# Kernel optimization log

Hardware: AMD Instinct MI355X
Metric: run time of the kernel (lower is better)

## Reference

```python
import jax, jax.numpy as jnp
import numpy as np

EMBED_DIM = 1024
HEADS = 16
D_HEAD = EMBED_DIM // HEADS
B, S = 4, 2048


def setup_inputs() -> dict:
    key = jax.random.key(0)
    ks = jax.random.split(key, 7)
    scale = 1.0 / np.sqrt(EMBED_DIM)
    inp = {
        "key": jax.random.normal(ks[0], (B, S, EMBED_DIM), jnp.float32),
        "query": jax.random.normal(ks[1], (B, S, EMBED_DIM), jnp.float32),
        "value": jax.random.normal(ks[2], (B, S, EMBED_DIM), jnp.float32),
        # causal boolean mask, broadcastable to [B, H, S, S]
        "mask": jnp.tril(jnp.ones((S, S), dtype=bool))[None, None, :, :] * jnp.ones((B, 1, 1, 1), dtype=bool),
        # nn.Linear weights, stored torch-style as [out_features, in_features]
        "Wq": jax.random.normal(ks[3], (EMBED_DIM, EMBED_DIM), jnp.float32) * scale,
        "Wk": jax.random.normal(ks[4], (EMBED_DIM, EMBED_DIM), jnp.float32) * scale,
        "Wv": jax.random.normal(ks[5], (EMBED_DIM, EMBED_DIM), jnp.float32) * scale,
        "Wo": jax.random.normal(ks[6], (EMBED_DIM, EMBED_DIM), jnp.float32) * scale,
    }
    return inp


def reference(key, query, value, mask, Wq, Wk, Wv, Wo):
    # projections (nn.Linear, bias=False): x @ W.T
    q = query @ Wq.T                                    # [B,S,E]
    k = key @ Wk.T
    v = value @ Wv.T
    # split heads -> [B,H,S,d]
    def split(x):
        return x.reshape(B, S, HEADS, D_HEAD).transpose(0, 2, 1, 3)
    q, k, v = split(q), split(k), split(v)
    # scaled dot-product scores [B,H,S,S]
    scores = jnp.einsum("bhqd,bhkd->bhqk", q, k) / np.sqrt(D_HEAD).astype(np.float32)
    scores = jnp.where(mask, scores, jnp.float32(-1e9))
    attn = jax.nn.softmax(scores, axis=-1)
    # attention output, merge heads
    out = jnp.einsum("bhqk,bhkd->bhqd", attn, v)        # [B,H,S,d]
    out = out.transpose(0, 2, 1, 3).reshape(B, S, EMBED_DIM)
    return out @ Wo.T
```

## Files before the change

kernel.cpp:

```cpp
#include <hip/hip_runtime.h>

#define SEQ 2048
#define EMBED 1024
#define DHEAD 64

typedef _Float16 h8 __attribute__((ext_vector_type(8)));
typedef _Float16 h4 __attribute__((ext_vector_type(4)));
typedef float f4 __attribute__((ext_vector_type(4)));
typedef unsigned int u32;

__device__ __forceinline__ void gload_lds16(const void* g, void* l) {
    __builtin_amdgcn_global_load_lds(
        (const __attribute__((address_space(1))) u32*)g,
        (__attribute__((address_space(3))) u32*)l, 16, 0, 0);
}

__global__ __launch_bounds__(256) void cvt_f16(
    const float* __restrict__ q, const float* __restrict__ k, const float* __restrict__ v,
    const float* __restrict__ wq, const float* __restrict__ wk, const float* __restrict__ wv,
    const float* __restrict__ wo,
    _Float16* __restrict__ q16, _Float16* __restrict__ k16, _Float16* __restrict__ v16,
    _Float16* __restrict__ wq16, _Float16* __restrict__ wk16, _Float16* __restrict__ wv16,
    _Float16* __restrict__ wo16)
{
    int bid = blockIdx.x;
    const float* src;
    _Float16* dst;
    float scale = 1.0f;
    size_t base;
    if (bid < 24576) {
        int seg = bid >> 13;
        base = (size_t)(bid & 8191) * 1024 + threadIdx.x * 4;
        src = seg == 0 ? q : seg == 1 ? k : v;
        dst = seg == 0 ? q16 : seg == 1 ? k16 : v16;
    } else {
        int wb = bid - 24576;
        int seg = wb >> 10;
        base = (size_t)(wb & 1023) * 1024 + threadIdx.x * 4;
        src = seg == 0 ? wq : seg == 1 ? wk : seg == 2 ? wv : wo;
        dst = seg == 0 ? wq16 : seg == 1 ? wk16 : seg == 2 ? wv16 : wo16;
        if (seg == 0) scale = 0.18033688011112042f;
    }
    float4 x = *(const float4*)(src + base);
    h4 y = { (_Float16)(x.x * scale), (_Float16)(x.y * scale),
             (_Float16)(x.z * scale), (_Float16)(x.w * scale) };
    *(h4*)(dst + base) = y;
}

__device__ __forceinline__ void gemm_core(const _Float16* __restrict__ A, const _Float16* __restrict__ W,
                                          int m0, int n0, int tid,
                                          _Float16* As, _Float16* Bs, f4 acc[4][4])
{
    const int lane = tid & 63, wave = tid >> 6;
    const int t16 = lane & 15, quad = lane >> 4;
    const int wm = (wave >> 1) * 64, wn = (wave & 1) * 64;
    const int wb = wave * 64;
    const int u0 = tid, u1 = tid + 256;
    const int r0 = u0 >> 2, c0 = u0 & 3;
    const int r1 = u1 >> 2, c1 = u1 & 3;
    const _Float16* ga0 = A + (size_t)(m0 + r0) * 1024 + c0 * 8;
    const _Float16* ga1 = A + (size_t)(m0 + r1) * 1024 + c1 * 8;
    const _Float16* gb0 = W + (size_t)(n0 + r0) * 1024 + c0 * 8;
    const _Float16* gb1 = W + (size_t)(n0 + r1) * 1024 + c1 * 8;
    _Float16* la0 = As + wb * 8;
    _Float16* la1 = As + (256 + wb) * 8;
    _Float16* lb0 = Bs + wb * 8;
    _Float16* lb1 = Bs + (256 + wb) * 8;

    for (int k0 = 0; k0 < 1024; k0 += 32) {
        __syncthreads();
        gload_lds16(ga0 + k0, la0);
        gload_lds16(ga1 + k0, la1);
        gload_lds16(gb0 + k0, lb0);
        gload_lds16(gb1 + k0, lb1);
        __syncthreads();
        h8 af[4], bf[4];
#pragma unroll
        for (int i = 0; i < 4; ++i)
            af[i] = *(const h8*)(As + (wm + i * 16 + t16) * 32 + quad * 8);
#pragma unroll
        for (int j = 0; j < 4; ++j)
            bf[j] = *(const h8*)(Bs + (wn + j * 16 + t16) * 32 + quad * 8);
#pragma unroll
        for (int i = 0; i < 4; ++i)
#pragma unroll
            for (int j = 0; j < 4; ++j)
                acc[i][j] = __builtin_amdgcn_mfma_f32_16x16x32_f16(af[i], bf[j], acc[i][j], 0, 0, 0);
    }
}

__global__ __launch_bounds__(256) void proj_qkv(
    const _Float16* __restrict__ q16, const _Float16* __restrict__ k16, const _Float16* __restrict__ v16,
    const _Float16* __restrict__ Wq, const _Float16* __restrict__ Wk, const _Float16* __restrict__ Wv,
    _Float16* __restrict__ Qh, _Float16* __restrict__ Kh, _Float16* __restrict__ Vt)
{
    __shared__ _Float16 As[4096], Bs[4096];
    const int tid = threadIdx.x;
    const int z = blockIdx.z;
    const _Float16 *A, *W;
    int m0, n0;
    if (z == 2) { A = Wv; W = v16; m0 = blockIdx.y * 128; n0 = blockIdx.x * 128; }
    else if (z == 0) { A = q16; W = Wq; m0 = blockIdx.x * 128; n0 = blockIdx.y * 128; }
    else { A = k16; W = Wk; m0 = blockIdx.x * 128; n0 = blockIdx.y * 128; }

    f4 acc[4][4];
    const f4 z4 = {0.f, 0.f, 0.f, 0.f};
#pragma unroll
    for (int i = 0; i < 4; ++i)
#pragma unroll
        for (int j = 0; j < 4; ++j) acc[i][j] = z4;

    gemm_core(A, W, m0, n0, tid, As, Bs, acc);

    const int lane = tid & 63, wave = tid >> 6;
    const int t16 = lane & 15, quad = lane >> 4;
    const int wm = (wave >> 1) * 64, wn = (wave & 1) * 64;
#pragma unroll
    for (int i = 0; i < 4; ++i)
#pragma unroll
        for (int j = 0; j < 4; ++j)
#pragma unroll
            for (int reg = 0; reg < 4; ++reg) {
                int gm = m0 + wm + i * 16 + quad * 4 + reg;
                int gn = n0 + wn + j * 16 + t16;
                float vv = acc[i][j][reg];
                if (z < 2) {
                    int b = gm >> 11, s = gm & 2047, h = gn >> 6, dd = gn & 63;
                    _Float16* dst = (z == 0) ? Qh : Kh;
                    dst[(((size_t)(b * 16 + h) * SEQ) + s) * DHEAD + dd] = (_Float16)vv;
                } else {
                    int h = gm >> 6, dd = gm & 63, b = gn >> 11, s = gn & 2047;
                    Vt[(((size_t)(b * 16 + h) * DHEAD) + dd) * SEQ + s] = (_Float16)vv;
                }
            }
}

__global__ __launch_bounds__(256) void attn2(
    const _Float16* __restrict__ Qh, const _Float16* __restrict__ Kh,
    const _Float16* __restrict__ Vt, _Float16* __restrict__ Ob)
{
    __shared__ _Float16 KVs[2][2][4096];
    __shared__ float Ps[64 * 68];
    const int tid = threadIdx.x;
    const int lane = tid & 63, wave = tid >> 6;
    const int t16 = lane & 15, quad = lane >> 4;
    const int bh = blockIdx.x;
    const int b = bh >> 4, h = bh & 15;
    const int qb = (gridDim.y - 1) - blockIdx.y;
    const int q0 = qb * 64;
    const int nt = qb + 1;

    const _Float16* Qp = Qh + (size_t)bh * SEQ * DHEAD;
    const _Float16* Kp = Kh + (size_t)bh * SEQ * DHEAD;
    const _Float16* Vp = Vt + (size_t)bh * DHEAD * SEQ;

    h8 qf0 = *(const h8*)(Qp + (size_t)(q0 + wave * 16 + t16) * 64 + quad * 8);
    h8 qf1 = *(const h8*)(Qp + (size_t)(q0 + wave * 16 + t16) * 64 + 32 + quad * 8);

    const int wb = wave * 64;
    const int sr0 = tid >> 3,          sc0 = (tid & 7) ^ (sr0 & 7);
    const int sr1 = (tid + 256) >> 3,  sc1 = ((tid + 256) & 7) ^ (sr1 & 7);

#define STAGE(jt, bufi)                                                                     \
    do {                                                                                    \
        gload_lds16(Kp + (size_t)((jt) * 64 + sr0) * 64 + sc0 * 8, &KVs[bufi][0][wb * 8]);  \
        gload_lds16(Kp + (size_t)((jt) * 64 + sr1) * 64 + sc1 * 8, &KVs[bufi][0][(256 + wb) * 8]); \
        gload_lds16(Vp + (size_t)sr0 * SEQ + (jt) * 64 + sc0 * 8, &KVs[bufi][1][wb * 8]);   \
        gload_lds16(Vp + (size_t)sr1 * SEQ + (jt) * 64 + sc1 * 8, &KVs[bufi][1][(256 + wb) * 8]); \
    } while (0)

    STAGE(0, 0);
    __syncthreads();

    float m_r[4] = {-1e30f, -1e30f, -1e30f, -1e30f};
    float l_r[4] = {0.f, 0.f, 0.f, 0.f};
    f4 o_acc[4];
    const f4 z4 = {0.f, 0.f, 0.f, 0.f};
#pragma unroll
    for (int dt = 0; dt < 4; ++dt) o_acc[dt] = z4;

    for (int jt = 0; jt < nt; ++jt) {
        const int buf = jt & 1;
        if (jt + 1 < nt) STAGE(jt + 1, buf ^ 1);
        const _Float16* Ks = KVs[buf][0];
        const _Float16* Vs = KVs[buf][1];

        f4 s_acc[4];
#pragma unroll
        for (int j4 = 0; j4 < 4; ++j4) s_acc[j4] = z4;
#pragma unroll
        for (int j4 = 0; j4 < 4; ++j4) {
            int row = j4 * 16 + t16, rx = row & 7;
            h8 kf0 = *(const h8*)(Ks + (row * 8 + (quad ^ rx)) * 8);
            h8 kf1 = *(const h8*)(Ks + (row * 8 + ((quad + 4) ^ rx)) * 8);
            s_acc[j4] = __builtin_amdgcn_mfma_f32_16x16x32_f16(qf0, kf0, s_acc[j4], 0, 0, 0);
            s_acc[j4] = __builtin_amdgcn_mfma_f32_16x16x32_f16(qf1, kf1, s_acc[j4], 0, 0, 0);
        }

        if (jt == nt - 1) {
#pragma unroll
            for (int j4 = 0; j4 < 4; ++j4) {
                int jg = jt * 64 + j4 * 16 + t16;
#pragma unroll
                for (int reg = 0; reg < 4; ++reg) {
                    int ig = q0 + wave * 16 + quad * 4 + reg;
                    if (jg > ig) s_acc[j4][reg] = -1e30f;
                }
            }
        }

        float mrow[4];
#pragma unroll
        for (int reg = 0; reg < 4; ++reg)
            mrow[reg] = fmaxf(fmaxf(s_acc[0][reg], s_acc[1][reg]),
                              fmaxf(s_acc[2][reg], s_acc[3][reg]));
#pragma unroll
        for (int off = 1; off < 16; off <<= 1)
#pragma unroll
            for (int reg = 0; reg < 4; ++reg)
                mrow[reg] = fmaxf(mrow[reg], __shfl_xor(mrow[reg], off, 64));

        float alpha[4];
#pragma unroll
        for (int reg = 0; reg < 4; ++reg) {
            float mn = fmaxf(m_r[reg], mrow[reg]);
            alpha[reg] = __builtin_amdgcn_exp2f(m_r[reg] - mn);
            m_r[reg] = mn;
        }
        float rsum[4] = {0.f, 0.f, 0.f, 0.f};
#pragma unroll
        for (int j4 = 0; j4 < 4; ++j4)
#pragma unroll
            for (int reg = 0; reg < 4; ++reg) {
                float p = __builtin_amdgcn_exp2f(s_acc[j4][reg] - m_r[reg]);
                s_acc[j4][reg] = p;
                rsum[reg] += p;
            }
#pragma unroll
        for (int off = 1; off < 16; off <<= 1)
#pragma unroll
            for (int reg = 0; reg < 4; ++reg)
                rsum[reg] += __shfl_xor(rsum[reg], off, 64);
#pragma unroll
        for (int reg = 0; reg < 4; ++reg)
            l_r[reg] = l_r[reg] * alpha[reg] + rsum[reg];

#pragma unroll
        for (int j4 = 0; j4 < 4; ++j4)
#pragma unroll
            for (int reg = 0; reg < 4; ++reg)
                Ps[(wave * 16 + quad * 4 + reg) * 68 + j4 * 16 + t16] = s_acc[j4][reg];

#pragma unroll
        for (int dt = 0; dt < 4; ++dt)
#pragma unroll
            for (int reg = 0; reg < 4; ++reg)
                o_acc[dt][reg] *= alpha[reg];

        const float* Pr = Ps + (wave * 16 + t16) * 68;
        float4 p0 = *(const float4*)(Pr + quad * 8);
        float4 p1 = *(const float4*)(Pr + quad * 8 + 4);
        float4 p2 = *(const float4*)(Pr + 32 + quad * 8);
        float4 p3 = *(const float4*)(Pr + 32 + quad * 8 + 4);
        h8 pf0 = { (_Float16)p0.x, (_Float16)p0.y, (_Float16)p0.z, (_Float16)p0.w,
                   (_Float16)p1.x, (_Float16)p1.y, (_Float16)p1.z, (_Float16)p1.w };
        h8 pf1 = { (_Float16)p2.x, (_Float16)p2.y, (_Float16)p2.z, (_Float16)p2.w,
                   (_Float16)p3.x, (_Float16)p3.y, (_Float16)p3.z, (_Float16)p3.w };

#pragma unroll
        for (int dt = 0; dt < 4; ++dt) {
            int row = dt * 16 + t16, rx = row & 7;
            h8 vf0 = *(const h8*)(Vs + (row * 8 + (quad ^ rx)) * 8);
            h8 vf1 = *(const h8*)(Vs + (row * 8 + ((quad + 4) ^ rx)) * 8);
            o_acc[dt] = __builtin_amdgcn_mfma_f32_16x16x32_f16(pf0, vf0, o_acc[dt], 0, 0, 0);
            o_acc[dt] = __builtin_amdgcn_mfma_f32_16x16x32_f16(pf1, vf1, o_acc[dt], 0, 0, 0);
        }
        __syncthreads();
    }

#pragma unroll
    for (int reg = 0; reg < 4; ++reg) {
        float inv = __builtin_amdgcn_rcpf(l_r[reg]);
        int s = q0 + wave * 16 + quad * 4 + reg;
#pragma unroll
        for (int dt = 0; dt < 4; ++dt)
            Ob[((size_t)(b * SEQ + s)) * EMBED + h * DHEAD + dt * 16 + t16] =
                (_Float16)(o_acc[dt][reg] * inv);
    }
}

__global__ __launch_bounds__(256) void proj_out(
    const _Float16* __restrict__ A, const _Float16* __restrict__ Wo, float* __restrict__ out)
{
    __shared__ _Float16 As[4096], Bs[4096];
    const int tid = threadIdx.x;
    const int m0 = blockIdx.x * 128, n0 = blockIdx.y * 128;
    f4 acc[4][4];
    const f4 z4 = {0.f, 0.f, 0.f, 0.f};
#pragma unroll
    for (int i = 0; i < 4; ++i)
#pragma unroll
        for (int j = 0; j < 4; ++j) acc[i][j] = z4;

    gemm_core(A, Wo, m0, n0, tid, As, Bs, acc);

    const int lane = tid & 63, wave = tid >> 6;
    const int t16 = lane & 15, quad = lane >> 4;
    const int wm = (wave >> 1) * 64, wn = (wave & 1) * 64;
#pragma unroll
    for (int i = 0; i < 4; ++i)
#pragma unroll
        for (int j = 0; j < 4; ++j)
#pragma unroll
            for (int reg = 0; reg < 4; ++reg) {
                int gm = m0 + wm + i * 16 + quad * 4 + reg;
                int gn = n0 + wn + j * 16 + t16;
                out[(size_t)gm * EMBED + gn] = acc[i][j][reg];
            }
}

extern "C" void kernel_launch(void* const* d_in, const int* in_sizes, int n_in,
                              void* d_out, int out_size, void* d_ws, size_t ws_size,
                              hipStream_t stream) {
    const float* key   = (const float*)d_in[0];
    const float* query = (const float*)d_in[1];
    const float* value = (const float*)d_in[2];
    const float* Wq = (const float*)d_in[4];
    const float* Wk = (const float*)d_in[5];
    const float* Wv = (const float*)d_in[6];
    const float* Wo = (const float*)d_in[7];

    char* ws = (char*)d_ws;
    _Float16* v16  = (_Float16*)(ws);
    _Float16* Wq16 = (_Float16*)(ws + (16u << 20));
    _Float16* Wk16 = (_Float16*)(ws + (18u << 20));
    _Float16* Wv16 = (_Float16*)(ws + (20u << 20));
    _Float16* Wo16 = (_Float16*)(ws + (22u << 20));
    _Float16* Qh   = (_Float16*)(ws + (24u << 20));
    _Float16* Kh   = (_Float16*)(ws + (40u << 20));
    _Float16* Vt   = (_Float16*)(ws + (56u << 20));
    _Float16* Ob   = v16;
    _Float16* q16 = (_Float16*)d_out;
    _Float16* k16 = (_Float16*)d_out + 8388608;

    dim3 blk(256);
    cvt_f16<<<dim3(28672), blk, 0, stream>>>(query, key, value, Wq, Wk, Wv, Wo,
                                             q16, k16, v16, Wq16, Wk16, Wv16, Wo16);
    proj_qkv<<<dim3(64, 8, 3), blk, 0, stream>>>(q16, k16, v16, Wq16, Wk16, Wv16, Qh, Kh, Vt);
    attn2<<<dim3(64, 32), blk, 0, stream>>>(Qh, Kh, Vt, Ob);
    proj_out<<<dim3(64, 8), blk, 0, stream>>>(Ob, Wo16, (float*)d_out);
}
```

Measured before the change: 389.5 us.

## Rewrite attention kernel with 128-row query tiles and transposed S=K·Q MFMA

The attention kernel now processes 128 query rows per block, with each wave handling two 16-row query sub-tiles. This halves K/V tile loads per query and doubles MFMA work per LDS fetch. Scores are computed as K·Q so the row softmax needs only two cross-lane shuffles, and P is exchanged through a small per-wave fp16 LDS buffer instead of a padded fp32 tile. Output is staged in LDS for 16-byte global stores. The grid halves to 1024 blocks, which may hurt load balance on the causal triangle, and it adds more registers.

```diff
diff --git a/kernel.cpp b/kernel.cpp
--- a/kernel.cpp
+++ b/kernel.cpp
@@ -135,158 +135,185 @@
             }
 }
 
-__global__ __launch_bounds__(256) void attn2(
+__global__ __launch_bounds__(256) void attn3(
     const _Float16* __restrict__ Qh, const _Float16* __restrict__ Kh,
     const _Float16* __restrict__ Vt, _Float16* __restrict__ Ob)
 {
-    __shared__ _Float16 KVs[2][2][4096];
-    __shared__ float Ps[64 * 68];
+    __shared__ _Float16 Kbuf[2][8][512];
+    __shared__ _Float16 Vbuf[2][8][512];
+    __shared__ _Float16 Pex[4][2][2][512];
+
     const int tid = threadIdx.x;
     const int lane = tid & 63, wave = tid >> 6;
     const int t16 = lane & 15, quad = lane >> 4;
     const int bh = blockIdx.x;
     const int b = bh >> 4, h = bh & 15;
     const int qb = (gridDim.y - 1) - blockIdx.y;
-    const int q0 = qb * 64;
-    const int nt = qb + 1;
+    const int q0 = qb * 128;
+    const int nqt = qb * 2 + 2;
 
     const _Float16* Qp = Qh + (size_t)bh * SEQ * DHEAD;
     const _Float16* Kp = Kh + (size_t)bh * SEQ * DHEAD;
     const _Float16* Vp = Vt + (size_t)bh * DHEAD * SEQ;
 
-    h8 qf0 = *(const h8*)(Qp + (size_t)(q0 + wave * 16 + t16) * 64 + quad * 8);
-    h8 qf1 = *(const h8*)(Qp + (size_t)(q0 + wave * 16 + t16) * 64 + 32 + quad * 8);
-
-    const int wb = wave * 64;
-    const int sr0 = tid >> 3,          sc0 = (tid & 7) ^ (sr0 & 7);
-    const int sr1 = (tid + 256) >> 3,  sc1 = ((tid + 256) & 7) ^ (sr1 & 7);
-
-#define STAGE(jt, bufi)                                                                     \
-    do {                                                                                    \
-        gload_lds16(Kp + (size_t)((jt) * 64 + sr0) * 64 + sc0 * 8, &KVs[bufi][0][wb * 8]);  \
-        gload_lds16(Kp + (size_t)((jt) * 64 + sr1) * 64 + sc1 * 8, &KVs[bufi][0][(256 + wb) * 8]); \
-        gload_lds16(Vp + (size_t)sr0 * SEQ + (jt) * 64 + sc0 * 8, &KVs[bufi][1][wb * 8]);   \
-        gload_lds16(Vp + (size_t)sr1 * SEQ + (jt) * 64 + sc1 * 8, &KVs[bufi][1][(256 + wb) * 8]); \
+    const int qlo[2] = { q0 + wave * 32, q0 + wave * 32 + 16 };
+    const int last0 = (qlo[0] + 15) >> 6;
+    const int last1 = (qlo[1] + 15) >> 6;
+
+    h8 qf[2][2];
+#pragma unroll
+    for (int qb2 = 0; qb2 < 2; ++qb2)
+#pragma unroll
+        for (int kc = 0; kc < 2; ++kc)
+            qf[qb2][kc] = *(const h8*)(Qp + (size_t)(qlo[qb2] + t16) * 64 + kc * 32 + quad * 8);
+
+    const _Float16* Kl = Kp + t16 * 64 + quad * 8;
+    const _Float16* Vl = Vp + t16 * 2048 + quad * 8;
+
+#define STAGE(jt_, bufi)                                                                  \
+    do {                                                                                  \
+        if (wave < 2) {                                                                   \
+            _Pragma("unroll")                                                             \
+            for (int i_ = 0; i_ < 4; ++i_) {                                              \
+                int g_ = wave * 4 + i_;                                                   \
+                gload_lds16(Kl + (jt_) * 4096 + (g_ >> 1) * 1024 + (g_ & 1) * 32,         \
+                            &Kbuf[bufi][g_][0]);                                          \
+            }                                                                             \
+        } else {                                                                          \
+            _Pragma("unroll")                                                             \
+            for (int i_ = 0; i_ < 4; ++i_) {                                              \
+                int g_ = (wave - 2) * 4 + i_;                                             \
+                gload_lds16(Vl + (g_ >> 1) * 32768 + (jt_) * 64 + (g_ & 1) * 32,          \
+                            &Vbuf[bufi][g_][0]);                                          \
+            }                                                                             \
+        }                                                                                 \
     } while (0)
 
     STAGE(0, 0);
     __syncthreads();
 
-    float m_r[4] = {-1e30f, -1e30f, -1e30f, -1e30f};
-    float l_r[4] = {0.f, 0.f, 0.f, 0.f};
-    f4 o_acc[4];
+    float mv[2] = {-1e30f, -1e30f};
+    float lv[2] = {0.f, 0.f};
+    f4 o_acc[2][4];
     const f4 z4 = {0.f, 0.f, 0.f, 0.f};
 #pragma unroll
-    for (int dt = 0; dt < 4; ++dt) o_acc[dt] = z4;
-
-    for (int jt = 0; jt < nt; ++jt) {
+    for (int qb2 = 0; qb2 < 2; ++qb2)
+#pragma unroll
+        for (int dt = 0; dt < 4; ++dt) o_acc[qb2][dt] = z4;
+
+    for (int jt = 0; jt < nqt; ++jt) {
         const int buf = jt & 1;
-        if (jt + 1 < nt) STAGE(jt + 1, buf ^ 1);
-        const _Float16* Ks = KVs[buf][0];
-        const _Float16* Vs = KVs[buf][1];
-
-        f4 s_acc[4];
-#pragma unroll
-        for (int j4 = 0; j4 < 4; ++j4) s_acc[j4] = z4;
-#pragma unroll
-        for (int j4 = 0; j4 < 4; ++j4) {
-            int row = j4 * 16 + t16, rx = row & 7;
-            h8 kf0 = *(const h8*)(Ks + (row * 8 + (quad ^ rx)) * 8);
-            h8 kf1 = *(const h8*)(Ks + (row * 8 + ((quad + 4) ^ rx)) * 8);
-            s_acc[j4] = __builtin_amdgcn_mfma_f32_16x16x32_f16(qf0, kf0, s_acc[j4], 0, 0, 0);
-            s_acc[j4] = __builtin_amdgcn_mfma_f32_16x16x32_f16(qf1, kf1, s_acc[j4], 0, 0, 0);
-        }
-
-        if (jt == nt - 1) {
+        if (jt + 1 < nqt) STAGE(jt + 1, buf ^ 1);
+
+        if (jt <= last1) {
+            f4 s0[4], s1[4];
 #pragma unroll
             for (int j4 = 0; j4 < 4; ++j4) {
-                int jg = jt * 64 + j4 * 16 + t16;
-#pragma unroll
-                for (int reg = 0; reg < 4; ++reg) {
-                    int ig = q0 + wave * 16 + quad * 4 + reg;
-                    if (jg > ig) s_acc[j4][reg] = -1e30f;
-                }
+                h8 kfa = *(const h8*)(&Kbuf[buf][j4 * 2 + 0][lane * 8]);
+                h8 kfb = *(const h8*)(&Kbuf[buf][j4 * 2 + 1][lane * 8]);
+                s1[j4] = __builtin_amdgcn_mfma_f32_16x16x32_f16(kfa, qf[1][0], z4, 0, 0, 0);
+                s1[j4] = __builtin_amdgcn_mfma_f32_16x16x32_f16(kfb, qf[1][1], s1[j4], 0, 0, 0);
+                s0[j4] = __builtin_amdgcn_mfma_f32_16x16x32_f16(kfa, qf[0][0], z4, 0, 0, 0);
+                s0[j4] = __builtin_amdgcn_mfma_f32_16x16x32_f16(kfb, qf[0][1], s0[j4], 0, 0, 0);
             }
-        }
-
-        float mrow[4];
-#pragma unroll
-        for (int reg = 0; reg < 4; ++reg)
-            mrow[reg] = fmaxf(fmaxf(s_acc[0][reg], s_acc[1][reg]),
-                              fmaxf(s_acc[2][reg], s_acc[3][reg]));
-#pragma unroll
-        for (int off = 1; off < 16; off <<= 1)
-#pragma unroll
-            for (int reg = 0; reg < 4; ++reg)
-                mrow[reg] = fmaxf(mrow[reg], __shfl_xor(mrow[reg], off, 64));
-
-        float alpha[4];
-#pragma unroll
-        for (int reg = 0; reg < 4; ++reg) {
-            float mn = fmaxf(m_r[reg], mrow[reg]);
-            alpha[reg] = __builtin_amdgcn_exp2f(m_r[reg] - mn);
-            m_r[reg] = mn;
-        }
-        float rsum[4] = {0.f, 0.f, 0.f, 0.f};
-#pragma unroll
-        for (int j4 = 0; j4 < 4; ++j4)
-#pragma unroll
-            for (int reg = 0; reg < 4; ++reg) {
-                float p = __builtin_amdgcn_exp2f(s_acc[j4][reg] - m_r[reg]);
-                s_acc[j4][reg] = p;
-                rsum[reg] += p;
+
+            auto softmax_store = [&](f4* s, int qb2) {
+                const int myq = qlo[qb2] + t16;
+                if ((jt << 6) + 63 > myq - t16 + 15 || true) {  }
+                if ((jt << 6) + 63 > qlo[qb2]) {
+#pragma unroll
+                    for (int j4 = 0; j4 < 4; ++j4)
+#pragma unroll
+                        for (int reg = 0; reg < 4; ++reg) {
+                            int kk = (jt << 6) + j4 * 16 + quad * 4 + reg;
+                            if (kk > myq) s[j4][reg] = -1e30f;
+                        }
+                }
+                float mr = s[0][0];
+#pragma unroll
+                for (int j4 = 0; j4 < 4; ++j4)
+#pragma unroll
+                    for (int reg = 0; reg < 4; ++reg) mr = fmaxf(mr, s[j4][reg]);
+                mr = fmaxf(mr, __shfl_xor(mr, 16, 64));
+                mr = fmaxf(mr, __shfl_xor(mr, 32, 64));
+                float mn = fmaxf(mv[qb2], mr);
+                float al = __builtin_amdgcn_exp2f(mv[qb2] - mn);
+                mv[qb2] = mn;
+                float rs = 0.f;
+#pragma unroll
+                for (int j4 = 0; j4 < 4; ++j4)
+#pragma unroll
+                    for (int reg = 0; reg < 4; ++reg) {
+                        float p = __builtin_amdgcn_exp2f(s[j4][reg] - mn);
+                        s[j4][reg] = p;
+                        rs += p;
+                    }
+                rs += __shfl_xor(rs, 16, 64);
+                rs += __shfl_xor(rs, 32, 64);
+                lv[qb2] = lv[qb2] * al + rs;
+#pragma unroll
+                for (int dt = 0; dt < 4; ++dt)
+#pragma unroll
+                    for (int reg = 0; reg < 4; ++reg) o_acc[qb2][dt][reg] *= al;
+#pragma unroll
+                for (int j4 = 0; j4 < 4; ++j4) {
+                    int Lt = (((j4 & 1) * 2 + (quad >> 1)) << 4) + t16;
+                    h4 ph = { (_Float16)s[j4][0], (_Float16)s[j4][1],
+                              (_Float16)s[j4][2], (_Float16)s[j4][3] };
+                    *(h4*)(&Pex[wave][qb2][j4 >> 1][Lt * 8 + (quad & 1) * 4]) = ph;
+                }
+            };
+
+            if (jt <= last0) {
+                softmax_store(s0, 0);
+                softmax_store(s1, 1);
+                h8 pb0a = *(const h8*)(&Pex[wave][0][0][lane * 8]);
+                h8 pb0b = *(const h8*)(&Pex[wave][0][1][lane * 8]);
+                h8 pb1a = *(const h8*)(&Pex[wave][1][0][lane * 8]);
+                h8 pb1b = *(const h8*)(&Pex[wave][1][1][lane * 8]);
+#pragma unroll
+                for (int dt = 0; dt < 4; ++dt) {
+                    h8 ava = *(const h8*)(&Vbuf[buf][dt * 2 + 0][lane * 8]);
+                    h8 avb = *(const h8*)(&Vbuf[buf][dt * 2 + 1][lane * 8]);
+                    o_acc[0][dt] = __builtin_amdgcn_mfma_f32_16x16x32_f16(ava, pb0a, o_acc[0][dt], 0, 0, 0);
+                    o_acc[0][dt] = __builtin_amdgcn_mfma_f32_16x16x32_f16(avb, pb0b, o_acc[0][dt], 0, 0, 0);
+                    o_acc[1][dt] = __builtin_amdgcn_mfma_f32_16x16x32_f16(ava, pb1a, o_acc[1][dt], 0, 0, 0);
+                    o_acc[1][dt] = __builtin_amdgcn_mfma_f32_16x16x32_f16(avb, pb1b, o_acc[1][dt], 0, 0, 0);
+                }
+            } else {
+                softmax_store(s1, 1);
+                h8 pb1a = *(const h8*)(&Pex[wave][1][0][lane * 8]);
+                h8 pb1b = *(const h8*)(&Pex[wave][1][1][lane * 8]);
+#pragma unroll
+                for (int dt = 0; dt < 4; ++dt) {
+                    h8 ava = *(const h8*)(&Vbuf[buf][dt * 2 + 0][lane * 8]);
+                    h8 avb = *(const h8*)(&Vbuf[buf][dt * 2 + 1][lane * 8]);
+                    o_acc[1][dt] = __builtin_amdgcn_mfma_f32_16x16x32_f16(ava, pb1a, o_acc[1][dt], 0, 0, 0);
+                    o_acc[1][dt] = __builtin_amdgcn_mfma_f32_16x16x32_f16(avb, pb1b, o_acc[1][dt], 0, 0, 0);
+                }
             }
-#pragma unroll
-        for (int off = 1; off < 16; off <<= 1)
-#pragma unroll
-            for (int reg = 0; reg < 4; ++reg)
-                rsum[reg] += __shfl_xor(rsum[reg], off, 64);
-#pragma unroll
-        for (int reg = 0; reg < 4; ++reg)
-            l_r[reg] = l_r[reg] * alpha[reg] + rsum[reg];
-
-#pragma unroll
-        for (int j4 = 0; j4 < 4; ++j4)
-#pragma unroll
-            for (int reg = 0; reg < 4; ++reg)
-                Ps[(wave * 16 + quad * 4 + reg) * 68 + j4 * 16 + t16] = s_acc[j4][reg];
-
-#pragma unroll
-        for (int dt = 0; dt < 4; ++dt)
-#pragma unroll
-            for (int reg = 0; reg < 4; ++reg)
-                o_acc[dt][reg] *= alpha[reg];
-
-        const float* Pr = Ps + (wave * 16 + t16) * 68;
-        float4 p0 = *(const float4*)(Pr + quad * 8);
-        float4 p1 = *(const float4*)(Pr + quad * 8 + 4);
-        float4 p2 = *(const float4*)(Pr + 32 + quad * 8);
-        float4 p3 = *(const float4*)(Pr + 32 + quad * 8 + 4);
-        h8 pf0 = { (_Float16)p0.x, (_Float16)p0.y, (_Float16)p0.z, (_Float16)p0.w,
-                   (_Float16)p1.x, (_Float16)p1.y, (_Float16)p1.z, (_Float16)p1.w };
-        h8 pf1 = { (_Float16)p2.x, (_Float16)p2.y, (_Float16)p2.z, (_Float16)p2.w,
-                   (_Float16)p3.x, (_Float16)p3.y, (_Float16)p3.z, (_Float16)p3.w };
-
-#pragma unroll
-        for (int dt = 0; dt < 4; ++dt) {
-            int row = dt * 16 + t16, rx = row & 7;
-            h8 vf0 = *(const h8*)(Vs + (row * 8 + (quad ^ rx)) * 8);
-            h8 vf1 = *(const h8*)(Vs + (row * 8 + ((quad + 4) ^ rx)) * 8);
-            o_acc[dt] = __builtin_amdgcn_mfma_f32_16x16x32_f16(pf0, vf0, o_acc[dt], 0, 0, 0);
-            o_acc[dt] = __builtin_amdgcn_mfma_f32_16x16x32_f16(pf1, vf1, o_acc[dt], 0, 0, 0);
         }
         __syncthreads();
     }
 
 #pragma unroll
-    for (int reg = 0; reg < 4; ++reg) {
-        float inv = __builtin_amdgcn_rcpf(l_r[reg]);
-        int s = q0 + wave * 16 + quad * 4 + reg;
-#pragma unroll
-        for (int dt = 0; dt < 4; ++dt)
-            Ob[((size_t)(b * SEQ + s)) * EMBED + h * DHEAD + dt * 16 + t16] =
-                (_Float16)(o_acc[dt][reg] * inv);
+    for (int qb2 = 0; qb2 < 2; ++qb2) {
+        float inv = __builtin_amdgcn_rcpf(lv[qb2]);
+        _Float16* ep = &Pex[wave][qb2][0][0];
+#pragma unroll
+        for (int dt = 0; dt < 4; ++dt) {
+            h4 ov = { (_Float16)(o_acc[qb2][dt][0] * inv), (_Float16)(o_acc[qb2][dt][1] * inv),
+                      (_Float16)(o_acc[qb2][dt][2] * inv), (_Float16)(o_acc[qb2][dt][3] * inv) };
+            *(h4*)(ep + t16 * 64 + dt * 16 + quad * 4) = ov;
+        }
+        h8 r0 = *(const h8*)(ep + t16 * 64 + quad * 8);
+        h8 r1 = *(const h8*)(ep + t16 * 64 + 32 + quad * 8);
+        int s = qlo[qb2] + t16;
+        _Float16* og = Ob + ((size_t)(b * SEQ + s)) * EMBED + h * DHEAD;
+        *(h8*)(og + quad * 8) = r0;
+        *(h8*)(og + 32 + quad * 8) = r1;
     }
+#undef STAGE
 }
 
 __global__ __launch_bounds__(256) void proj_out(
@@ -347,6 +374,6 @@
     cvt_f16<<<dim3(28672), blk, 0, stream>>>(query, key, value, Wq, Wk, Wv, Wo,
                                              q16, k16, v16, Wq16, Wk16, Wv16, Wo16);
     proj_qkv<<<dim3(64, 8, 3), blk, 0, stream>>>(q16, k16, v16, Wq16, Wk16, Wv16, Qh, Kh, Vt);
-    attn2<<<dim3(64, 32), blk, 0, stream>>>(Qh, Kh, Vt, Ob);
+    attn3<<<dim3(64, 16), blk, 0, stream>>>(Qh, Kh, Vt, Ob);
     proj_out<<<dim3(64, 8), blk, 0, stream>>>(Ob, Wo16, (float*)d_out);
 }
```

New measurement: 338.8 us. 13.0% less time.
